# Kernel tuning notes

Hardware: AMD Instinct MI355X
Metric: run time of the kernel (lower is better)

## Reference

```python
import jax, jax.numpy as jnp
import numpy as np

NEG_SLOPE = 0.2  # PyG GATConv default negative_slope


def setup_inputs() -> dict:
    key = jax.random.key(0)
    k_x, k_e, k_w, k_as, k_ad = jax.random.split(key, 5)
    B, F, N, D, E, L = 2, 16, 5000, 128, 40000, 3
    x = jax.random.normal(k_x, (B, F, N, D), dtype=jnp.float32)
    edge_index = jax.random.randint(k_e, (B, F, 2, E), 0, N, dtype=jnp.int64)
    Ws = jax.random.normal(k_w, (L, D, D), dtype=jnp.float32) / np.float32(np.sqrt(D))
    att_src = jax.random.normal(k_as, (L, D), dtype=jnp.float32) / np.float32(np.sqrt(D))
    att_dst = jax.random.normal(k_ad, (L, D), dtype=jnp.float32) / np.float32(np.sqrt(D))
    bias = jnp.zeros((L, D), dtype=jnp.float32)
    return {"x": x, "edge_index": edge_index, "Ws": Ws,
            "att_src": att_src, "att_dst": att_dst, "bias": bias}


def _gat_layer(h, src, dst, n, W, a_s, a_d, b):
    # h: [n, D] node features; src/dst: [E_tot] edge endpoints (self-loops included)
    h2 = h @ W                                   # [n, D] transformed features
    s = h2 @ a_s                                 # [n] per-node source score
    d = h2 @ a_d                                 # [n] per-node dest score
    e = jax.nn.leaky_relu(s[src] + d[dst], NEG_SLOPE)   # [E_tot] raw attention
    m = jax.lax.stop_gradient(jax.ops.segment_max(e, dst, num_segments=n))
    ex = jnp.exp(e - m[dst])                     # numerically stable softmax per dst
    denom = jax.ops.segment_sum(ex, dst, num_segments=n)
    alpha = ex / denom[dst]                      # [E_tot] normalized attention
    out = jax.ops.segment_sum(alpha[:, None] * h2[src], dst, num_segments=n) + b
    return jax.nn.relu(out)


def reference(x, edge_index, Ws, att_src, att_dst, bias):
    B, F, N, D = x.shape
    n = B * F * N
    h = x.reshape(n, D)
    # faithful to torch: (BF,2,E).view(2,-1) is a raw row-major reshape
    ei = edge_index.reshape(2, -1)
    loop = jnp.arange(n, dtype=ei.dtype)         # PyG GATConv adds self-loops
    src = jnp.concatenate([ei[0], loop])
    dst = jnp.concatenate([ei[1], loop])
    for l in range(Ws.shape[0]):                 # fixed small layer loop
        h = _gat_layer(h, src, dst, n, Ws[l], att_src[l], att_dst[l], bias[l])
    return h.reshape(B, F, N, D)
```

## Files before the change

kernel.cpp:

```cpp
#include <hip/hip_runtime.h>
#include <math.h>

#define NODES_TOTAL 160000
#define NODES_REAL  5000
#define D 128
#define NEG 0.2f
#define KP2 128
#define HL2 (128 * KP2)
#define WT2_L (2 * HL2)
#define CHUNK 16384

typedef unsigned short ushort_t;
typedef unsigned int uint_t;
typedef __attribute__((ext_vector_type(8))) __bf16 bf16x8;
typedef __attribute__((ext_vector_type(4))) float f32x4;
union BF8 { bf16x8 v; ushort_t u[8]; };

__device__ __forceinline__ void split2(float x, ushort_t& hi, ushort_t& lo) {
    unsigned u = __float_as_uint(x);
    hi = (ushort_t)(u >> 16);
    float hif = __uint_as_float(u & 0xffff0000u);
    lo = (ushort_t)(__float_as_uint(x - hif) >> 16);
}
__device__ __forceinline__ uint_t encmax(float f) {
    uint_t b = __float_as_uint(f);
    return b ^ ((uint_t)((int)b >> 31) | 0x80000000u);
}
__device__ __forceinline__ float decmax(uint_t u) {
    uint_t b = (u & 0x80000000u) ? (u ^ 0x80000000u) : ~u;
    return __uint_as_float(b);
}

__global__ void wsplit_kernel(const float* __restrict__ Ws, ushort_t* __restrict__ Wm,
                              int* __restrict__ counts, uint_t* __restrict__ gmaxu) {
    int gid = blockIdx.x * 256 + threadIdx.x;
    if (gid < NODES_REAL) counts[gid] = 0;
    if (gid < 3) gmaxu[gid] = 0u;
    int l  = blockIdx.x >> 3;
    int n  = (blockIdx.x & 7) * 16 + (threadIdx.x >> 4);
    int c8 = threadIdx.x & 15;
    int k0 = c8 * 8;
    const float* src = Ws + (size_t)l * D * D;
    union { ushort_t u[8]; uint4 v; } hi, lo;
    #pragma unroll
    for (int j = 0; j < 8; ++j) split2(src[(size_t)(k0 + j) * D + n], hi.u[j], lo.u[j]);
    int ct = n >> 4, m16 = n & 15, kc = c8 >> 2, qq = c8 & 3;
    int lane = qq * 16 + m16;
    ushort_t* d2 = Wm + (size_t)l * WT2_L + ((ct * 4 + kc) * 2 + 0) * 512 + lane * 8;
    *(uint4*)d2 = hi.v;
    *(uint4*)(d2 + 512) = lo.v;
}

__global__ __launch_bounds__(256)
void rank2_kernel(const int* __restrict__ ei, int* __restrict__ counts,
                  int* __restrict__ bases, ushort_t* __restrict__ rank16, int Eh) {
    __shared__ uint_t lc[NODES_REAL];
    int c = blockIdx.x, tid = threadIdx.x;
    for (int i = tid; i < NODES_REAL; i += 256) lc[i] = 0u;
    __syncthreads();
    int e0 = c * CHUNK;
    #pragma unroll 4
    for (int k = 0; k < CHUNK / 256; ++k) {
        int e = e0 + k * 256 + tid;
        if (e < Eh) {
            int d = ei[Eh + e];
            uint_t r = atomicAdd(&lc[d], 1u);
            rank16[e] = (ushort_t)r;
        }
    }
    __syncthreads();
    for (int i = tid; i < NODES_REAL; i += 256) {
        uint_t n = lc[i];
        if (n > 0u)
            bases[c * NODES_REAL + i] = atomicAdd(&counts[i], (int)n);
    }
}

__global__ void scan_kernel(const int* __restrict__ counts, int* __restrict__ offs) {
    __shared__ int sd[1024];
    int t = threadIdx.x;
    int pre[5]; int sum = 0;
    #pragma unroll
    for (int u = 0; u < 5; ++u) {
        int idx = t * 5 + u;
        int c = (idx < NODES_REAL) ? counts[idx] : 0;
        pre[u] = sum; sum += c;
    }
    sd[t] = sum;
    __syncthreads();
    int run = sum;
    for (int o = 1; o < 1024; o <<= 1) {
        int v = (t >= o) ? sd[t - o] : 0;
        __syncthreads();
        sd[t] += v;
        __syncthreads();
    }
    int excl = sd[t] - run;
    #pragma unroll
    for (int u = 0; u < 5; ++u) {
        int idx = t * 5 + u;
        if (idx < NODES_REAL) offs[idx] = excl + pre[u];
    }
    if (t == 1023) offs[NODES_REAL] = excl + run;
}

__global__ void scatter_det(const int* __restrict__ ei, const int* __restrict__ offs,
                            const int* __restrict__ bases,
                            const ushort_t* __restrict__ rank16, ushort_t* __restrict__ esrc,
                            int Eh) {
    int e = blockIdx.x * blockDim.x + threadIdx.x;
    if (e < Eh) {
        int s = ei[e];
        int d = ei[Eh + e];
        int c = e >> 14;
        esrc[offs[d] + bases[c * NODES_REAL + d] + (int)rank16[e]] = (ushort_t)s;
    }
}

__global__ __launch_bounds__(256, 2)
void mlp3_kernel(const float* __restrict__ x, const ushort_t* __restrict__ Wm,
                 const float* __restrict__ bs, float* __restrict__ out) {
    __shared__ float scr[2][2][16][132];
    int tid = threadIdx.x;
    int w = tid >> 6, lane = tid & 63, q = lane >> 4, m16 = lane & 15;
    int p = w >> 1, h = w & 1;
    int row0 = NODES_REAL + blockIdx.x * 64 + p * 32;

    float4 xa[2][4][2];
    #pragma unroll
    for (int rt = 0; rt < 2; ++rt) {
        int r = row0 + rt * 16 + m16;
        if (r > NODES_TOTAL - 1) r = NODES_TOTAL - 1;
        #pragma unroll
        for (int kc = 0; kc < 4; ++kc) {
            const float* gp = x + (size_t)r * D + kc * 32 + q * 8;
            xa[rt][kc][0] = *(const float4*)gp;
            xa[rt][kc][1] = *(const float4*)(gp + 4);
        }
    }

    f32x4 acc[2][4];
    #pragma unroll
    for (int l = 0; l < 3; ++l) {
        const ushort_t* Wml = Wm + (size_t)l * WT2_L;
        if (l > 0) __syncthreads();

        BF8 ahi[2][4], alo[2][4];
        #pragma unroll
        for (int rt = 0; rt < 2; ++rt)
            #pragma unroll
            for (int kc = 0; kc < 4; ++kc) {
                float4 v0, v1;
                if (l == 0) { v0 = xa[rt][kc][0]; v1 = xa[rt][kc][1]; }
                else {
                    const float* sp = &scr[p][rt][m16][kc * 32 + q * 8];
                    v0 = *(const float4*)sp; v1 = *(const float4*)(sp + 4);
                }
                float xv[8] = {v0.x, v0.y, v0.z, v0.w, v1.x, v1.y, v1.z, v1.w};
                #pragma unroll
                for (int j = 0; j < 8; ++j) split2(xv[j], ahi[rt][kc].u[j], alo[rt][kc].u[j]);
            }
        if (l > 0) __syncthreads();

        #pragma unroll
        for (int rt = 0; rt < 2; ++rt)
            #pragma unroll
            for (int ct = 0; ct < 4; ++ct) acc[rt][ct] = (f32x4){0.f, 0.f, 0.f, 0.f};

        #pragma unroll
        for (int ph = 0; ph < 2; ++ph) {
            int kc0 = ph * 2;
            bf16x8 bh[4][2], bl[4][2];
            #pragma unroll
            for (int ct = 0; ct < 4; ++ct)
                #pragma unroll
                for (int dk = 0; dk < 2; ++dk) {
                    const ushort_t* bp = Wml + (((h * 4 + ct) * 4 + (kc0 + dk)) * 2) * 512 + lane * 8;
                    bh[ct][dk] = *(const bf16x8*)bp;
                    bl[ct][dk] = *(const bf16x8*)(bp + 512);
                }
            #pragma unroll
            for (int dk = 0; dk < 2; ++dk)
                #pragma unroll
                for (int ct = 0; ct < 4; ++ct)
                    #pragma unroll
                    for (int rt = 0; rt < 2; ++rt) {
                        acc[rt][ct] = __builtin_amdgcn_mfma_f32_16x16x32_bf16(ahi[rt][kc0 + dk].v, bh[ct][dk], acc[rt][ct], 0, 0, 0);
                        acc[rt][ct] = __builtin_amdgcn_mfma_f32_16x16x32_bf16(ahi[rt][kc0 + dk].v, bl[ct][dk], acc[rt][ct], 0, 0, 0);
                        acc[rt][ct] = __builtin_amdgcn_mfma_f32_16x16x32_bf16(alo[rt][kc0 + dk].v, bh[ct][dk], acc[rt][ct], 0, 0, 0);
                    }
        }
        float bv[4];
        #pragma unroll
        for (int ct = 0; ct < 4; ++ct) bv[ct] = bs[l * D + (h * 4 + ct) * 16 + m16];
        #pragma unroll
        for (int rt = 0; rt < 2; ++rt)
            #pragma unroll
            for (int ct = 0; ct < 4; ++ct)
                #pragma unroll
                for (int reg = 0; reg < 4; ++reg)
                    scr[p][rt][q * 4 + reg][(h * 4 + ct) * 16 + m16] =
                        fmaxf(acc[rt][ct][reg] + bv[ct], 0.f);
    }
    __syncthreads();
    #pragma unroll
    for (int i = 0; i < 8; ++i) {
        int rowl = i * 2 + (lane >> 5);
        int grow = row0 + h * 16 + rowl;
        float4 v = *(const float4*)&scr[p][h][rowl][(lane & 31) * 4];
        if (grow < NODES_TOTAL)
            *(float4*)&out[(size_t)grow * D + (lane & 31) * 4] = v;
    }
}

__global__ __launch_bounds__(64, 2)
void gsmall_kernel(const float* __restrict__ hin, const ushort_t* __restrict__ Wm,
                   const float* __restrict__ a_s, const float* __restrict__ a_d,
                   float* __restrict__ h2, float* __restrict__ sv, float* __restrict__ dv,
                   uint_t* __restrict__ gmaxu) {
    int lane = threadIdx.x & 63, q = lane >> 4, m16 = lane & 15;
    int row0 = blockIdx.x * 16;
    float4 xa[4][2];
    {
        int r = row0 + m16;
        if (r > NODES_REAL - 1) r = NODES_REAL - 1;
        #pragma unroll
        for (int kc = 0; kc < 4; ++kc) {
            const float* gp = hin + (size_t)r * D + kc * 32 + q * 8;
            xa[kc][0] = *(const float4*)gp;
            xa[kc][1] = *(const float4*)(gp + 4);
        }
    }
    f32x4 acc[8];
    #pragma unroll
    for (int ct = 0; ct < 8; ++ct) acc[ct] = (f32x4){0.f, 0.f, 0.f, 0.f};

    #pragma unroll
    for (int kc = 0; kc < 4; ++kc) {
        BF8 ahi, alo;
        {
            float4 v0 = xa[kc][0], v1 = xa[kc][1];
            float xv[8] = {v0.x, v0.y, v0.z, v0.w, v1.x, v1.y, v1.z, v1.w};
            #pragma unroll
            for (int j = 0; j < 8; ++j) split2(xv[j], ahi.u[j], alo.u[j]);
        }
        bf16x8 bh[8], bl[8];
        #pragma unroll
        for (int ct = 0; ct < 8; ++ct) {
            const ushort_t* bp = Wm + ((ct * 4 + kc) * 2) * 512 + lane * 8;
            bh[ct] = *(const bf16x8*)bp;
            bl[ct] = *(const bf16x8*)(bp + 512);
        }
        #pragma unroll
        for (int ct = 0; ct < 8; ++ct) {
            acc[ct] = __builtin_amdgcn_mfma_f32_16x16x32_bf16(ahi.v, bh[ct], acc[ct], 0, 0, 0);
            acc[ct] = __builtin_amdgcn_mfma_f32_16x16x32_bf16(ahi.v, bl[ct], acc[ct], 0, 0, 0);
            acc[ct] = __builtin_amdgcn_mfma_f32_16x16x32_bf16(alo.v, bh[ct], acc[ct], 0, 0, 0);
        }
    }
    #pragma unroll
    for (int reg = 0; reg < 4; ++reg) {
        int grow = row0 + q * 4 + reg;
        if (grow < NODES_REAL) {
            #pragma unroll
            for (int ct = 0; ct < 8; ++ct)
                h2[(size_t)grow * D + ct * 16 + m16] = acc[ct][reg];
        }
    }
    float asv[8], adv[8];
    #pragma unroll
    for (int ct = 0; ct < 8; ++ct) { asv[ct] = a_s[ct * 16 + m16]; adv[ct] = a_d[ct * 16 + m16]; }
    #pragma unroll
    for (int reg = 0; reg < 4; ++reg) {
        float ps = 0.f, pd = 0.f;
        #pragma unroll
        for (int ct = 0; ct < 8; ++ct) {
            float v = acc[ct][reg];
            ps += v * asv[ct]; pd += v * adv[ct];
        }
        #pragma unroll
        for (int o = 1; o < 16; o <<= 1) { ps += __shfl_xor(ps, o); pd += __shfl_xor(pd, o); }
        int grow = row0 + q * 4 + reg;
        if (m16 == 0 && grow < NODES_REAL) {
            sv[grow] = ps; dv[grow] = pd;
            atomicMax(gmaxu, encmax(ps));
        }
    }
}

__global__ __launch_bounds__(256)
void agg_kernel(const float* __restrict__ h2, const float* __restrict__ sv,
                const float* __restrict__ dv, const int* __restrict__ offs,
                const ushort_t* __restrict__ esrc, const float* __restrict__ bias,
                float* __restrict__ out, const uint_t* __restrict__ gmaxu) {
    __shared__ float2 pair_l[512];
    __shared__ float2 red[4][64];
    __shared__ float lexs[4];
    int tid = threadIdx.x, w = tid >> 6, lane = tid & 63;
    int i = blockIdx.x;
    int start = offs[i], end = offs[i + 1];
    float d_i = dv[i];
    float gm = decmax(*gmaxu) + d_i;
    float m = gm > 0.f ? gm : NEG * gm;
    const float2* h2v = (const float2*)h2;
    float ax0 = 0.f, ay0 = 0.f, ax1 = 0.f, ay1 = 0.f;
    float ax2 = 0.f, ay2 = 0.f, ax3 = 0.f, ay3 = 0.f, exs = 0.f;

    for (int tile = start; tile < end; tile += 512) {
        int tcnt = min(512, end - tile);
        __syncthreads();
        #pragma unroll
        for (int hh = 0; hh < 2; ++hh) {
            int j = hh * 256 + tid;
            if (j < tcnt) {
                int s = (int)esrc[tile + j];
                float sc = sv[s] + d_i;
                sc = sc > 0.f ? sc : NEG * sc;
                float ex = __expf(sc - m);
                exs += ex;
                pair_l[j] = make_float2(ex, __uint_as_float((uint_t)s));
            }
        }
        __syncthreads();
        for (int j0 = w * 64; j0 < tcnt; j0 += 256) {
            int jend = min(j0 + 64, tcnt);
            int j = j0;
            for (; j + 4 <= jend; j += 4) {
                float2 p0 = pair_l[j],     p1 = pair_l[j + 1];
                float2 p2 = pair_l[j + 2], p3 = pair_l[j + 3];
                float2 v0 = h2v[(size_t)__float_as_uint(p0.y) * 64 + lane];
                float2 v1 = h2v[(size_t)__float_as_uint(p1.y) * 64 + lane];
                float2 v2 = h2v[(size_t)__float_as_uint(p2.y) * 64 + lane];
                float2 v3 = h2v[(size_t)__float_as_uint(p3.y) * 64 + lane];
                ax0 += p0.x * v0.x; ay0 += p0.x * v0.y;
                ax1 += p1.x * v1.x; ay1 += p1.x * v1.y;
                ax2 += p2.x * v2.x; ay2 += p2.x * v2.y;
                ax3 += p3.x * v3.x; ay3 += p3.x * v3.y;
            }
            for (; j < jend; ++j) {
                float2 p0 = pair_l[j];
                float2 v0 = h2v[(size_t)__float_as_uint(p0.y) * 64 + lane];
                ax0 += p0.x * v0.x; ay0 += p0.x * v0.y;
            }
        }
    }
    float ax = (ax0 + ax1) + (ax2 + ax3);
    float ay = (ay0 + ay1) + (ay2 + ay3);
    #pragma unroll
    for (int o = 1; o < 64; o <<= 1) exs += __shfl_xor(exs, o);
    __syncthreads();
    red[w][lane] = make_float2(ax, ay);
    if (lane == 0) lexs[w] = exs;
    __syncthreads();
    if (w == 0) {
        float2 r1 = red[1][lane], r2 = red[2][lane], r3 = red[3][lane];
        ax += r1.x + r2.x + r3.x;
        ay += r1.y + r2.y + r3.y;
        float exst = lexs[0] + lexs[1] + lexs[2] + lexs[3];
        float scf = sv[i] + d_i; scf = scf > 0.f ? scf : NEG * scf;
        float exf = __expf(scf - m);
        float2 hv = h2v[(size_t)i * 64 + lane];
        ax += exf * hv.x; ay += exf * hv.y;
        float rd = 1.f / (exst + exf);
        float2 b2 = *(const float2*)&bias[2 * lane];
        float2 o2 = make_float2(fmaxf(ax * rd + b2.x, 0.f), fmaxf(ay * rd + b2.y, 0.f));
        *(float2*)&out[(size_t)i * D + 2 * lane] = o2;
    }
}

extern "C" void kernel_launch(void* const* d_in, const int* in_sizes, int n_in,
                              void* d_out, int out_size, void* d_ws, size_t ws_size,
                              hipStream_t stream) {
    const float* x   = (const float*)d_in[0];
    const int*   ei  = (const int*)d_in[1];
    const float* Ws  = (const float*)d_in[2];
    const float* as_ = (const float*)d_in[3];
    const float* ad_ = (const float*)d_in[4];
    const float* bs  = (const float*)d_in[5];
    float* out = (float*)d_out;
    int Eh = in_sizes[1] / 2;
    int nchunks = (Eh + CHUNK - 1) / CHUNK;

    char* ws = (char*)d_ws;
    float*    h2     = (float*)ws;
    float*    bufS   = (float*)(ws + 2560000);
    float*    sv     = (float*)(ws + 5120000);
    float*    dv     = (float*)(ws + 5140000);
    int*      counts = (int*)  (ws + 5160000);
    int*      offs   = (int*)  (ws + 5180000);
    ushort_t* rank16 = (ushort_t*)(ws + 5200016);
    ushort_t* esrc   = (ushort_t*)(ws + 7760016);
    ushort_t* Wm     = (ushort_t*)(ws + 10320016);
    uint_t*   gmaxu  = (uint_t*)(ws + 10528912);
    int*      bases  = (int*)h2;

    wsplit_kernel<<<24, 256, 0, stream>>>(Ws, Wm, counts, gmaxu);
    rank2_kernel<<<nchunks, 256, 0, stream>>>(ei, counts, bases, rank16, Eh);
    scan_kernel<<<1, 1024, 0, stream>>>(counts, offs);
    scatter_det<<<(Eh + 255) / 256, 256, 0, stream>>>(ei, offs, bases, rank16, esrc, Eh);

    mlp3_kernel<<<(NODES_TOTAL - NODES_REAL + 63) / 64, 256, 0, stream>>>(x, Wm, bs, out);

    for (int l = 0; l < 3; ++l) {
        const float* hin = (l == 0) ? x : bufS;
        float* hout = (l == 2) ? out : bufS;
        gsmall_kernel<<<(NODES_REAL + 15) / 16, 64, 0, stream>>>(
            hin, Wm + (size_t)l * WT2_L, as_ + l * D, ad_ + l * D, h2, sv, dv, gmaxu + l);
        agg_kernel<<<NODES_REAL, 256, 0, stream>>>(
            h2, sv, dv, offs, esrc, bs + l * D, hout, gmaxu + l);
    }
}
```

Before: 481.2 us.

## Fuse graph build and three GAT layers into a persistent grid-synced megakernel

Replaces the separate rank, scan, scatter, per-layer transform and aggregation launches with one persistent kernel of 1024 blocks. The phases are separated by a software grid barrier built on a global atomic counter. Layer-0 feature transform now runs alongside the CSR ranking phase. The aim is to remove launch gaps and kernel tails across about ten small dependent kernels. In exchange it depends on all 1024 blocks being resident at once, because otherwise the spin barrier deadlocks, and it adds barrier spin cost.

```diff
diff --git a/kernel.cpp b/kernel.cpp
--- a/kernel.cpp
+++ b/kernel.cpp
@@ -9,6 +9,7 @@
 #define HL2 (128 * KP2)
 #define WT2_L (2 * HL2)
 #define CHUNK 16384
+#define MEGA_NB 1024
 
 typedef unsigned short ushort_t;
 typedef unsigned int uint_t;
@@ -31,11 +32,24 @@
     return __uint_as_float(b);
 }
 
+__device__ __forceinline__ void grid_sync(uint_t* cnt, uint_t target) {
+    __syncthreads();
+    if (threadIdx.x == 0) {
+        __threadfence();
+        atomicAdd(cnt, 1u);
+        while (*(volatile uint_t*)cnt < target) __builtin_amdgcn_s_sleep(2);
+        __threadfence();
+    }
+    __syncthreads();
+}
+
 __global__ void wsplit_kernel(const float* __restrict__ Ws, ushort_t* __restrict__ Wm,
-                              int* __restrict__ counts, uint_t* __restrict__ gmaxu) {
+                              int* __restrict__ counts, uint_t* __restrict__ gmaxu,
+                              uint_t* __restrict__ sync_cnt) {
     int gid = blockIdx.x * 256 + threadIdx.x;
     if (gid < NODES_REAL) counts[gid] = 0;
     if (gid < 3) gmaxu[gid] = 0u;
+    if (gid == 3) *sync_cnt = 0u;
     int l  = blockIdx.x >> 3;
     int n  = (blockIdx.x & 7) * 16 + (threadIdx.x >> 4);
     int c8 = threadIdx.x & 15;
@@ -49,72 +63,6 @@
     ushort_t* d2 = Wm + (size_t)l * WT2_L + ((ct * 4 + kc) * 2 + 0) * 512 + lane * 8;
     *(uint4*)d2 = hi.v;
     *(uint4*)(d2 + 512) = lo.v;
-}
-
-__global__ __launch_bounds__(256)
-void rank2_kernel(const int* __restrict__ ei, int* __restrict__ counts,
-                  int* __restrict__ bases, ushort_t* __restrict__ rank16, int Eh) {
-    __shared__ uint_t lc[NODES_REAL];
-    int c = blockIdx.x, tid = threadIdx.x;
-    for (int i = tid; i < NODES_REAL; i += 256) lc[i] = 0u;
-    __syncthreads();
-    int e0 = c * CHUNK;
-    #pragma unroll 4
-    for (int k = 0; k < CHUNK / 256; ++k) {
-        int e = e0 + k * 256 + tid;
-        if (e < Eh) {
-            int d = ei[Eh + e];
-            uint_t r = atomicAdd(&lc[d], 1u);
-            rank16[e] = (ushort_t)r;
-        }
-    }
-    __syncthreads();
-    for (int i = tid; i < NODES_REAL; i += 256) {
-        uint_t n = lc[i];
-        if (n > 0u)
-            bases[c * NODES_REAL + i] = atomicAdd(&counts[i], (int)n);
-    }
-}
-
-__global__ void scan_kernel(const int* __restrict__ counts, int* __restrict__ offs) {
-    __shared__ int sd[1024];
-    int t = threadIdx.x;
-    int pre[5]; int sum = 0;
-    #pragma unroll
-    for (int u = 0; u < 5; ++u) {
-        int idx = t * 5 + u;
-        int c = (idx < NODES_REAL) ? counts[idx] : 0;
-        pre[u] = sum; sum += c;
-    }
-    sd[t] = sum;
-    __syncthreads();
-    int run = sum;
-    for (int o = 1; o < 1024; o <<= 1) {
-        int v = (t >= o) ? sd[t - o] : 0;
-        __syncthreads();
-        sd[t] += v;
-        __syncthreads();
-    }
-    int excl = sd[t] - run;
-    #pragma unroll
-    for (int u = 0; u < 5; ++u) {
-        int idx = t * 5 + u;
-        if (idx < NODES_REAL) offs[idx] = excl + pre[u];
-    }
-    if (t == 1023) offs[NODES_REAL] = excl + run;
-}
-
-__global__ void scatter_det(const int* __restrict__ ei, const int* __restrict__ offs,
-                            const int* __restrict__ bases,
-                            const ushort_t* __restrict__ rank16, ushort_t* __restrict__ esrc,
-                            int Eh) {
-    int e = blockIdx.x * blockDim.x + threadIdx.x;
-    if (e < Eh) {
-        int s = ei[e];
-        int d = ei[Eh + e];
-        int c = e >> 14;
-        esrc[offs[d] + bases[c * NODES_REAL + d] + (int)rank16[e]] = (ushort_t)s;
-    }
 }
 
 __global__ __launch_bounds__(256, 2)
@@ -213,49 +161,43 @@
     }
 }
 
-__global__ __launch_bounds__(64, 2)
-void gsmall_kernel(const float* __restrict__ hin, const ushort_t* __restrict__ Wm,
-                   const float* __restrict__ a_s, const float* __restrict__ a_d,
-                   float* __restrict__ h2, float* __restrict__ sv, float* __restrict__ dv,
-                   uint_t* __restrict__ gmaxu) {
-    int lane = threadIdx.x & 63, q = lane >> 4, m16 = lane & 15;
-    int row0 = blockIdx.x * 16;
-    float4 xa[4][2];
-    {
-        int r = row0 + m16;
-        if (r > NODES_REAL - 1) r = NODES_REAL - 1;
-        #pragma unroll
-        for (int kc = 0; kc < 4; ++kc) {
-            const float* gp = hin + (size_t)r * D + kc * 32 + q * 8;
-            xa[kc][0] = *(const float4*)gp;
-            xa[kc][1] = *(const float4*)(gp + 4);
-        }
-    }
+__device__ __forceinline__ void gsmall_wave(const float* __restrict__ hin,
+        const ushort_t* __restrict__ Wml, const float* __restrict__ a_s,
+        const float* __restrict__ a_d, float* __restrict__ h2,
+        float* __restrict__ sv, float* __restrict__ dv, uint_t* __restrict__ gmax,
+        int row0, int lane) {
+    int q = lane >> 4, m16 = lane & 15;
+    int rr = row0 + m16; if (rr > NODES_REAL - 1) rr = NODES_REAL - 1;
     f32x4 acc[8];
     #pragma unroll
     for (int ct = 0; ct < 8; ++ct) acc[ct] = (f32x4){0.f, 0.f, 0.f, 0.f};
-
     #pragma unroll
     for (int kc = 0; kc < 4; ++kc) {
+        const float* gp = hin + (size_t)rr * D + kc * 32 + q * 8;
+        float4 v0 = *(const float4*)gp, v1 = *(const float4*)(gp + 4);
         BF8 ahi, alo;
         {
-            float4 v0 = xa[kc][0], v1 = xa[kc][1];
             float xv[8] = {v0.x, v0.y, v0.z, v0.w, v1.x, v1.y, v1.z, v1.w};
             #pragma unroll
             for (int j = 0; j < 8; ++j) split2(xv[j], ahi.u[j], alo.u[j]);
         }
-        bf16x8 bh[8], bl[8];
-        #pragma unroll
-        for (int ct = 0; ct < 8; ++ct) {
-            const ushort_t* bp = Wm + ((ct * 4 + kc) * 2) * 512 + lane * 8;
-            bh[ct] = *(const bf16x8*)bp;
-            bl[ct] = *(const bf16x8*)(bp + 512);
-        }
-        #pragma unroll
-        for (int ct = 0; ct < 8; ++ct) {
-            acc[ct] = __builtin_amdgcn_mfma_f32_16x16x32_bf16(ahi.v, bh[ct], acc[ct], 0, 0, 0);
-            acc[ct] = __builtin_amdgcn_mfma_f32_16x16x32_bf16(ahi.v, bl[ct], acc[ct], 0, 0, 0);
-            acc[ct] = __builtin_amdgcn_mfma_f32_16x16x32_bf16(alo.v, bh[ct], acc[ct], 0, 0, 0);
+        #pragma unroll
+        for (int cth = 0; cth < 2; ++cth) {
+            bf16x8 bh[4], bl[4];
+            #pragma unroll
+            for (int c4 = 0; c4 < 4; ++c4) {
+                int ct = cth * 4 + c4;
+                const ushort_t* bp = Wml + ((ct * 4 + kc) * 2) * 512 + lane * 8;
+                bh[c4] = *(const bf16x8*)bp;
+                bl[c4] = *(const bf16x8*)(bp + 512);
+            }
+            #pragma unroll
+            for (int c4 = 0; c4 < 4; ++c4) {
+                int ct = cth * 4 + c4;
+                acc[ct] = __builtin_amdgcn_mfma_f32_16x16x32_bf16(ahi.v, bh[c4], acc[ct], 0, 0, 0);
+                acc[ct] = __builtin_amdgcn_mfma_f32_16x16x32_bf16(ahi.v, bl[c4], acc[ct], 0, 0, 0);
+                acc[ct] = __builtin_amdgcn_mfma_f32_16x16x32_bf16(alo.v, bh[c4], acc[ct], 0, 0, 0);
+            }
         }
     }
     #pragma unroll
@@ -283,21 +225,17 @@
         int grow = row0 + q * 4 + reg;
         if (m16 == 0 && grow < NODES_REAL) {
             sv[grow] = ps; dv[grow] = pd;
-            atomicMax(gmaxu, encmax(ps));
-        }
-    }
-}
-
-__global__ __launch_bounds__(256)
-void agg_kernel(const float* __restrict__ h2, const float* __restrict__ sv,
-                const float* __restrict__ dv, const int* __restrict__ offs,
-                const ushort_t* __restrict__ esrc, const float* __restrict__ bias,
-                float* __restrict__ out, const uint_t* __restrict__ gmaxu) {
-    __shared__ float2 pair_l[512];
-    __shared__ float2 red[4][64];
-    __shared__ float lexs[4];
-    int tid = threadIdx.x, w = tid >> 6, lane = tid & 63;
-    int i = blockIdx.x;
+            atomicMax(gmax, encmax(ps));
+        }
+    }
+}
+
+__device__ __forceinline__ void agg_dst(int i, const float* __restrict__ h2,
+        const float* __restrict__ sv, const float* __restrict__ dv,
+        const int* __restrict__ offs, const ushort_t* __restrict__ esrc,
+        const float* __restrict__ bias, float* __restrict__ hout,
+        const uint_t* __restrict__ gmaxu, int w, int lane, int tid,
+        float2* pair_l, float2 (*red)[64], float* lexs) {
     int start = offs[i], end = offs[i + 1];
     float d_i = dv[i];
     float gm = decmax(*gmaxu) + d_i;
@@ -305,7 +243,6 @@
     const float2* h2v = (const float2*)h2;
     float ax0 = 0.f, ay0 = 0.f, ax1 = 0.f, ay1 = 0.f;
     float ax2 = 0.f, ay2 = 0.f, ax3 = 0.f, ay3 = 0.f, exs = 0.f;
-
     for (int tile = start; tile < end; tile += 512) {
         int tcnt = min(512, end - tile);
         __syncthreads();
@@ -364,8 +301,116 @@
         float rd = 1.f / (exst + exf);
         float2 b2 = *(const float2*)&bias[2 * lane];
         float2 o2 = make_float2(fmaxf(ax * rd + b2.x, 0.f), fmaxf(ay * rd + b2.y, 0.f));
-        *(float2*)&out[(size_t)i * D + 2 * lane] = o2;
-    }
+        *(float2*)&hout[(size_t)i * D + 2 * lane] = o2;
+    }
+}
+
+__global__ __launch_bounds__(256, 4)
+void mega_kernel(const float* __restrict__ x, const ushort_t* __restrict__ Wm,
+                 const float* __restrict__ as_, const float* __restrict__ ad_,
+                 const float* __restrict__ bs, const int* __restrict__ ei,
+                 float* __restrict__ h2, float* __restrict__ bufS,
+                 float* __restrict__ sv, float* __restrict__ dv,
+                 int* __restrict__ counts, int* __restrict__ offs,
+                 ushort_t* __restrict__ rank16, ushort_t* __restrict__ esrc,
+                 uint_t* __restrict__ gmaxu, float* __restrict__ out,
+                 uint_t* __restrict__ sync_cnt, int Eh, int nchunks) {
+    __shared__ uint_t lc[NODES_REAL];
+    __shared__ float2 pair_l[512];
+    __shared__ float2 red[4][64];
+    __shared__ float lexs[4];
+    __shared__ int sd2[256];
+    int b = blockIdx.x, tid = threadIdx.x;
+    int w = tid >> 6, lane = tid & 63;
+    uint_t NB = gridDim.x;
+    int* bases = (int*)bufS;
+
+    if (b < nchunks) {
+        for (int i2 = tid; i2 < NODES_REAL; i2 += 256) lc[i2] = 0u;
+        __syncthreads();
+        int e0 = b * CHUNK;
+        #pragma unroll 4
+        for (int k = 0; k < CHUNK / 256; ++k) {
+            int e = e0 + k * 256 + tid;
+            if (e < Eh) {
+                int d = ei[Eh + e];
+                uint_t r = atomicAdd(&lc[d], 1u);
+                rank16[e] = (ushort_t)r;
+            }
+        }
+        __syncthreads();
+        for (int i2 = tid; i2 < NODES_REAL; i2 += 256) {
+            uint_t n = lc[i2];
+            if (n > 0u)
+                bases[b * NODES_REAL + i2] = atomicAdd(&counts[i2], (int)n);
+        }
+    } else {
+        int gw = (b - nchunks) * 4 + w;
+        if (gw * 16 < NODES_REAL)
+            gsmall_wave(x, Wm, as_, ad_, h2, sv, dv, gmaxu + 0, gw * 16, lane);
+    }
+    uint_t tgt = NB; grid_sync(sync_cnt, tgt);
+
+    if (b == 0) {
+        int t = tid;
+        int pre[20]; int sum = 0;
+        #pragma unroll
+        for (int u = 0; u < 20; ++u) {
+            int idx = t * 20 + u;
+            int c = (idx < NODES_REAL) ? counts[idx] : 0;
+            pre[u] = sum; sum += c;
+        }
+        sd2[t] = sum;
+        __syncthreads();
+        int run = sum;
+        for (int o = 1; o < 256; o <<= 1) {
+            int v = (t >= o) ? sd2[t - o] : 0;
+            __syncthreads();
+            sd2[t] += v;
+            __syncthreads();
+        }
+        int excl = sd2[t] - run;
+        #pragma unroll
+        for (int u = 0; u < 20; ++u) {
+            int idx = t * 20 + u;
+            if (idx < NODES_REAL) offs[idx] = excl + pre[u];
+        }
+        if (t == 255) offs[NODES_REAL] = excl + run;
+    }
+    tgt += NB; grid_sync(sync_cnt, tgt);
+
+    for (int e = b * 256 + tid; e < Eh; e += (int)NB * 256) {
+        int s = ei[e];
+        int d = ei[Eh + e];
+        int c = e >> 14;
+        esrc[offs[d] + bases[c * NODES_REAL + d] + (int)rank16[e]] = (ushort_t)s;
+    }
+    tgt += NB; grid_sync(sync_cnt, tgt);
+
+    for (int i = b; i < NODES_REAL; i += (int)NB)
+        agg_dst(i, h2, sv, dv, offs, esrc, bs + 0 * D, bufS, gmaxu + 0, w, lane, tid, pair_l, red, lexs);
+    tgt += NB; grid_sync(sync_cnt, tgt);
+
+    {
+        int gw = b * 4 + w;
+        if (gw * 16 < NODES_REAL)
+            gsmall_wave(bufS, Wm + WT2_L, as_ + D, ad_ + D, h2, sv, dv, gmaxu + 1, gw * 16, lane);
+    }
+    tgt += NB; grid_sync(sync_cnt, tgt);
+
+    for (int i = b; i < NODES_REAL; i += (int)NB)
+        agg_dst(i, h2, sv, dv, offs, esrc, bs + D, bufS, gmaxu + 1, w, lane, tid, pair_l, red, lexs);
+    tgt += NB; grid_sync(sync_cnt, tgt);
+
+    {
+        int gw = b * 4 + w;
+        if (gw * 16 < NODES_REAL)
+            gsmall_wave(bufS, Wm + 2 * WT2_L, as_ + 2 * D, ad_ + 2 * D, h2, sv, dv, gmaxu + 2, gw * 16, lane);
+    }
+    tgt += NB; grid_sync(sync_cnt, tgt);
+
+    for (int i = b; i < NODES_REAL; i += (int)NB)
+        agg_dst(i, h2, sv, dv, offs, esrc, bs + 2 * D, out, gmaxu + 2, w, lane, tid, pair_l, red, lexs);
 }
 
 extern "C" void kernel_launch(void* const* d_in, const int* in_sizes, int n_in,
@@ -392,21 +437,13 @@
     ushort_t* esrc   = (ushort_t*)(ws + 7760016);
     ushort_t* Wm     = (ushort_t*)(ws + 10320016);
     uint_t*   gmaxu  = (uint_t*)(ws + 10528912);
-    int*      bases  = (int*)h2;
-
-    wsplit_kernel<<<24, 256, 0, stream>>>(Ws, Wm, counts, gmaxu);
-    rank2_kernel<<<nchunks, 256, 0, stream>>>(ei, counts, bases, rank16, Eh);
-    scan_kernel<<<1, 1024, 0, stream>>>(counts, offs);
-    scatter_det<<<(Eh + 255) / 256, 256, 0, stream>>>(ei, offs, bases, rank16, esrc, Eh);
+    uint_t*   sync_cnt = (uint_t*)(ws + 10528928);
+
+    wsplit_kernel<<<24, 256, 0, stream>>>(Ws, Wm, counts, gmaxu, sync_cnt);
 
     mlp3_kernel<<<(NODES_TOTAL - NODES_REAL + 63) / 64, 256, 0, stream>>>(x, Wm, bs, out);
 
-    for (int l = 0; l < 3; ++l) {
-        const float* hin = (l == 0) ? x : bufS;
-        float* hout = (l == 2) ? out : bufS;
-        gsmall_kernel<<<(NODES_REAL + 15) / 16, 64, 0, stream>>>(
-            hin, Wm + (size_t)l * WT2_L, as_ + l * D, ad_ + l * D, h2, sv, dv, gmaxu + l);
-        agg_kernel<<<NODES_REAL, 256, 0, stream>>>(
-            h2, sv, dv, offs, esrc, bs + l * D, hout, gmaxu + l);
-    }
-}
+    mega_kernel<<<MEGA_NB, 256, 0, stream>>>(x, Wm, as_, ad_, bs, ei, h2, bufS, sv, dv,
+                                             counts, offs, rank16, esrc, gmaxu, out,
+                                             sync_cnt, Eh, nchunks);
+}
```

New measurement: 1.429 ms. 2.97x slower.

## Overlap MLP for isolated nodes with graph layers via combined kernels

Applied to the files above, without the earlier changes.

The large MLP over nodes without edges is split into three slices, and each slice is launched in the same grid as one layer's aggregation blocks. This lets the independent dense work fill the GPU while the latency-bound per-node aggregation runs. The edge-rank kernel is also merged with the layer-0 feature transform, and the rank bases buffer moves to bufS so it does not clash with h2. The cost is higher LDS and register use in the merged kernels, which may lower occupancy, and the blocks become unevenly sized.

```diff
diff --git a/kernel.cpp b/kernel.cpp
--- a/kernel.cpp
+++ b/kernel.cpp
@@ -51,80 +51,13 @@
     *(uint4*)(d2 + 512) = lo.v;
 }
 
-__global__ __launch_bounds__(256)
-void rank2_kernel(const int* __restrict__ ei, int* __restrict__ counts,
-                  int* __restrict__ bases, ushort_t* __restrict__ rank16, int Eh) {
-    __shared__ uint_t lc[NODES_REAL];
-    int c = blockIdx.x, tid = threadIdx.x;
-    for (int i = tid; i < NODES_REAL; i += 256) lc[i] = 0u;
-    __syncthreads();
-    int e0 = c * CHUNK;
-    #pragma unroll 4
-    for (int k = 0; k < CHUNK / 256; ++k) {
-        int e = e0 + k * 256 + tid;
-        if (e < Eh) {
-            int d = ei[Eh + e];
-            uint_t r = atomicAdd(&lc[d], 1u);
-            rank16[e] = (ushort_t)r;
-        }
-    }
-    __syncthreads();
-    for (int i = tid; i < NODES_REAL; i += 256) {
-        uint_t n = lc[i];
-        if (n > 0u)
-            bases[c * NODES_REAL + i] = atomicAdd(&counts[i], (int)n);
-    }
-}
-
-__global__ void scan_kernel(const int* __restrict__ counts, int* __restrict__ offs) {
-    __shared__ int sd[1024];
-    int t = threadIdx.x;
-    int pre[5]; int sum = 0;
-    #pragma unroll
-    for (int u = 0; u < 5; ++u) {
-        int idx = t * 5 + u;
-        int c = (idx < NODES_REAL) ? counts[idx] : 0;
-        pre[u] = sum; sum += c;
-    }
-    sd[t] = sum;
-    __syncthreads();
-    int run = sum;
-    for (int o = 1; o < 1024; o <<= 1) {
-        int v = (t >= o) ? sd[t - o] : 0;
-        __syncthreads();
-        sd[t] += v;
-        __syncthreads();
-    }
-    int excl = sd[t] - run;
-    #pragma unroll
-    for (int u = 0; u < 5; ++u) {
-        int idx = t * 5 + u;
-        if (idx < NODES_REAL) offs[idx] = excl + pre[u];
-    }
-    if (t == 1023) offs[NODES_REAL] = excl + run;
-}
-
-__global__ void scatter_det(const int* __restrict__ ei, const int* __restrict__ offs,
-                            const int* __restrict__ bases,
-                            const ushort_t* __restrict__ rank16, ushort_t* __restrict__ esrc,
-                            int Eh) {
-    int e = blockIdx.x * blockDim.x + threadIdx.x;
-    if (e < Eh) {
-        int s = ei[e];
-        int d = ei[Eh + e];
-        int c = e >> 14;
-        esrc[offs[d] + bases[c * NODES_REAL + d] + (int)rank16[e]] = (ushort_t)s;
-    }
-}
-
-__global__ __launch_bounds__(256, 2)
-void mlp3_kernel(const float* __restrict__ x, const ushort_t* __restrict__ Wm,
-                 const float* __restrict__ bs, float* __restrict__ out) {
-    __shared__ float scr[2][2][16][132];
-    int tid = threadIdx.x;
+__device__ __forceinline__ void mlp3_body(const float* __restrict__ x,
+        const ushort_t* __restrict__ Wm, const float* __restrict__ bs,
+        float* __restrict__ out, int row_base, int bid, int tid,
+        float (*scr)[2][16][132]) {
     int w = tid >> 6, lane = tid & 63, q = lane >> 4, m16 = lane & 15;
     int p = w >> 1, h = w & 1;
-    int row0 = NODES_REAL + blockIdx.x * 64 + p * 32;
+    int row0 = row_base + bid * 64 + p * 32;
 
     float4 xa[2][4][2];
     #pragma unroll
@@ -213,49 +146,43 @@
     }
 }
 
-__global__ __launch_bounds__(64, 2)
-void gsmall_kernel(const float* __restrict__ hin, const ushort_t* __restrict__ Wm,
-                   const float* __restrict__ a_s, const float* __restrict__ a_d,
-                   float* __restrict__ h2, float* __restrict__ sv, float* __restrict__ dv,
-                   uint_t* __restrict__ gmaxu) {
-    int lane = threadIdx.x & 63, q = lane >> 4, m16 = lane & 15;
-    int row0 = blockIdx.x * 16;
-    float4 xa[4][2];
-    {
-        int r = row0 + m16;
-        if (r > NODES_REAL - 1) r = NODES_REAL - 1;
-        #pragma unroll
-        for (int kc = 0; kc < 4; ++kc) {
-            const float* gp = hin + (size_t)r * D + kc * 32 + q * 8;
-            xa[kc][0] = *(const float4*)gp;
-            xa[kc][1] = *(const float4*)(gp + 4);
-        }
-    }
+__device__ __forceinline__ void gsmall_wave(const float* __restrict__ hin,
+        const ushort_t* __restrict__ Wml, const float* __restrict__ a_s,
+        const float* __restrict__ a_d, float* __restrict__ h2,
+        float* __restrict__ sv, float* __restrict__ dv, uint_t* __restrict__ gmax,
+        int row0, int lane) {
+    int q = lane >> 4, m16 = lane & 15;
+    int rr = row0 + m16; if (rr > NODES_REAL - 1) rr = NODES_REAL - 1;
     f32x4 acc[8];
     #pragma unroll
     for (int ct = 0; ct < 8; ++ct) acc[ct] = (f32x4){0.f, 0.f, 0.f, 0.f};
-
     #pragma unroll
     for (int kc = 0; kc < 4; ++kc) {
+        const float* gp = hin + (size_t)rr * D + kc * 32 + q * 8;
+        float4 v0 = *(const float4*)gp, v1 = *(const float4*)(gp + 4);
         BF8 ahi, alo;
         {
-            float4 v0 = xa[kc][0], v1 = xa[kc][1];
             float xv[8] = {v0.x, v0.y, v0.z, v0.w, v1.x, v1.y, v1.z, v1.w};
             #pragma unroll
             for (int j = 0; j < 8; ++j) split2(xv[j], ahi.u[j], alo.u[j]);
         }
-        bf16x8 bh[8], bl[8];
-        #pragma unroll
-        for (int ct = 0; ct < 8; ++ct) {
-            const ushort_t* bp = Wm + ((ct * 4 + kc) * 2) * 512 + lane * 8;
-            bh[ct] = *(const bf16x8*)bp;
-            bl[ct] = *(const bf16x8*)(bp + 512);
-        }
-        #pragma unroll
-        for (int ct = 0; ct < 8; ++ct) {
-            acc[ct] = __builtin_amdgcn_mfma_f32_16x16x32_bf16(ahi.v, bh[ct], acc[ct], 0, 0, 0);
-            acc[ct] = __builtin_amdgcn_mfma_f32_16x16x32_bf16(ahi.v, bl[ct], acc[ct], 0, 0, 0);
-            acc[ct] = __builtin_amdgcn_mfma_f32_16x16x32_bf16(alo.v, bh[ct], acc[ct], 0, 0, 0);
+        #pragma unroll
+        for (int cth = 0; cth < 2; ++cth) {
+            bf16x8 bh[4], bl[4];
+            #pragma unroll
+            for (int c4 = 0; c4 < 4; ++c4) {
+                int ct = cth * 4 + c4;
+                const ushort_t* bp = Wml + ((ct * 4 + kc) * 2) * 512 + lane * 8;
+                bh[c4] = *(const bf16x8*)bp;
+                bl[c4] = *(const bf16x8*)(bp + 512);
+            }
+            #pragma unroll
+            for (int c4 = 0; c4 < 4; ++c4) {
+                int ct = cth * 4 + c4;
+                acc[ct] = __builtin_amdgcn_mfma_f32_16x16x32_bf16(ahi.v, bh[c4], acc[ct], 0, 0, 0);
+                acc[ct] = __builtin_amdgcn_mfma_f32_16x16x32_bf16(ahi.v, bl[c4], acc[ct], 0, 0, 0);
+                acc[ct] = __builtin_amdgcn_mfma_f32_16x16x32_bf16(alo.v, bh[c4], acc[ct], 0, 0, 0);
+            }
         }
     }
     #pragma unroll
@@ -283,21 +210,17 @@
         int grow = row0 + q * 4 + reg;
         if (m16 == 0 && grow < NODES_REAL) {
             sv[grow] = ps; dv[grow] = pd;
-            atomicMax(gmaxu, encmax(ps));
-        }
-    }
-}
-
-__global__ __launch_bounds__(256)
-void agg_kernel(const float* __restrict__ h2, const float* __restrict__ sv,
-                const float* __restrict__ dv, const int* __restrict__ offs,
-                const ushort_t* __restrict__ esrc, const float* __restrict__ bias,
-                float* __restrict__ out, const uint_t* __restrict__ gmaxu) {
-    __shared__ float2 pair_l[512];
-    __shared__ float2 red[4][64];
-    __shared__ float lexs[4];
-    int tid = threadIdx.x, w = tid >> 6, lane = tid & 63;
-    int i = blockIdx.x;
+            atomicMax(gmax, encmax(ps));
+        }
+    }
+}
+
+__device__ __forceinline__ void agg_dst(int i, const float* __restrict__ h2,
+        const float* __restrict__ sv, const float* __restrict__ dv,
+        const int* __restrict__ offs, const ushort_t* __restrict__ esrc,
+        const float* __restrict__ bias, float* __restrict__ hout,
+        const uint_t* __restrict__ gmaxu, int w, int lane, int tid,
+        float2* pair_l, float2 (*red)[64], float* lexs) {
     int start = offs[i], end = offs[i + 1];
     float d_i = dv[i];
     float gm = decmax(*gmaxu) + d_i;
@@ -305,7 +228,6 @@
     const float2* h2v = (const float2*)h2;
     float ax0 = 0.f, ay0 = 0.f, ax1 = 0.f, ay1 = 0.f;
     float ax2 = 0.f, ay2 = 0.f, ax3 = 0.f, ay3 = 0.f, exs = 0.f;
-
     for (int tile = start; tile < end; tile += 512) {
         int tcnt = min(512, end - tile);
         __syncthreads();
@@ -364,8 +286,115 @@
         float rd = 1.f / (exst + exf);
         float2 b2 = *(const float2*)&bias[2 * lane];
         float2 o2 = make_float2(fmaxf(ax * rd + b2.x, 0.f), fmaxf(ay * rd + b2.y, 0.f));
-        *(float2*)&out[(size_t)i * D + 2 * lane] = o2;
-    }
+        *(float2*)&hout[(size_t)i * D + 2 * lane] = o2;
+    }
+}
+
+__global__ __launch_bounds__(256, 4)
+void comboA_kernel(const int* __restrict__ ei, int* __restrict__ counts,
+                   int* __restrict__ bases, ushort_t* __restrict__ rank16,
+                   int Eh, int nchunks,
+                   const float* __restrict__ x, const ushort_t* __restrict__ Wm,
+                   const float* __restrict__ as_, const float* __restrict__ ad_,
+                   float* __restrict__ h2, float* __restrict__ sv,
+                   float* __restrict__ dv, uint_t* __restrict__ gmaxu) {
+    __shared__ uint_t lc[NODES_REAL];
+    int b = blockIdx.x, tid = threadIdx.x;
+    if (b < nchunks) {
+        for (int i2 = tid; i2 < NODES_REAL; i2 += 256) lc[i2] = 0u;
+        __syncthreads();
+        int e0 = b * CHUNK;
+        #pragma unroll 4
+        for (int k = 0; k < CHUNK / 256; ++k) {
+            int e = e0 + k * 256 + tid;
+            if (e < Eh) {
+                int d = ei[Eh + e];
+                uint_t r = atomicAdd(&lc[d], 1u);
+                rank16[e] = (ushort_t)r;
+            }
+        }
+        __syncthreads();
+        for (int i2 = tid; i2 < NODES_REAL; i2 += 256) {
+            uint_t n = lc[i2];
+            if (n > 0u)
+                bases[b * NODES_REAL + i2] = atomicAdd(&counts[i2], (int)n);
+        }
+    } else {
+        int gw = (b - nchunks) * 4 + (tid >> 6);
+        if (gw * 16 < NODES_REAL)
+            gsmall_wave(x, Wm, as_, ad_, h2, sv, dv, gmaxu + 0, gw * 16, tid & 63);
+    }
+}
+
+__global__ void scan_kernel(const int* __restrict__ counts, int* __restrict__ offs) {
+    __shared__ int sd[1024];
+    int t = threadIdx.x;
+    int pre[5]; int sum = 0;
+    #pragma unroll
+    for (int u = 0; u < 5; ++u) {
+        int idx = t * 5 + u;
+        int c = (idx < NODES_REAL) ? counts[idx] : 0;
+        pre[u] = sum; sum += c;
+    }
+    sd[t] = sum;
+    __syncthreads();
+    int run = sum;
+    for (int o = 1; o < 1024; o <<= 1) {
+        int v = (t >= o) ? sd[t - o] : 0;
+        __syncthreads();
+        sd[t] += v;
+        __syncthreads();
+    }
+    int excl = sd[t] - run;
+    #pragma unroll
+    for (int u = 0; u < 5; ++u) {
+        int idx = t * 5 + u;
+        if (idx < NODES_REAL) offs[idx] = excl + pre[u];
+    }
+    if (t == 1023) offs[NODES_REAL] = excl + run;
+}
+
+__global__ void scatter_det(const int* __restrict__ ei, const int* __restrict__ offs,
+                            const int* __restrict__ bases,
+                            const ushort_t* __restrict__ rank16, ushort_t* __restrict__ esrc,
+                            int Eh) {
+    int e = blockIdx.x * blockDim.x + threadIdx.x;
+    if (e < Eh) {
+        int s = ei[e];
+        int d = ei[Eh + e];
+        int c = e >> 14;
+        esrc[offs[d] + bases[c * NODES_REAL + d] + (int)rank16[e]] = (ushort_t)s;
+    }
+}
+
+__global__ __launch_bounds__(256, 2)
+void combo_kernel(const float* __restrict__ x, const ushort_t* __restrict__ Wm,
+                  const float* __restrict__ bs, float* __restrict__ out,
+                  int mlp_nb, int mlp_row_base,
+                  const float* __restrict__ h2, const float* __restrict__ sv,
+                  const float* __restrict__ dv, const int* __restrict__ offs,
+                  const ushort_t* __restrict__ esrc, const float* __restrict__ bias_l,
+                  float* __restrict__ hout, const uint_t* __restrict__ gmaxu_l) {
+    __shared__ float scr[2][2][16][132];
+    __shared__ float2 pair_l[512];
+    __shared__ float2 red[4][64];
+    __shared__ float lexs[4];
+    int b = blockIdx.x, tid = threadIdx.x;
+    if (b < mlp_nb) {
+        mlp3_body(x, Wm, bs, out, mlp_row_base, b, tid, scr);
+    } else {
+        int i = b - mlp_nb;
+        agg_dst(i, h2, sv, dv, offs, esrc, bias_l, hout, gmaxu_l,
+                tid >> 6, tid & 63, tid, pair_l, red, lexs);
+    }
+}
+
+__global__ __launch_bounds__(64, 2)
+void gsmall_kernel(const float* __restrict__ hin, const ushort_t* __restrict__ Wm,
+                   const float* __restrict__ a_s, const float* __restrict__ a_d,
+                   float* __restrict__ h2, float* __restrict__ sv, float* __restrict__ dv,
+                   uint_t* __restrict__ gmaxu) {
+    gsmall_wave(hin, Wm, a_s, a_d, h2, sv, dv, gmaxu, blockIdx.x * 16, threadIdx.x & 63);
 }
 
 extern "C" void kernel_launch(void* const* d_in, const int* in_sizes, int n_in,
@@ -392,21 +421,28 @@
     ushort_t* esrc   = (ushort_t*)(ws + 7760016);
     ushort_t* Wm     = (ushort_t*)(ws + 10320016);
     uint_t*   gmaxu  = (uint_t*)(ws + 10528912);
-    int*      bases  = (int*)h2;
+    int*      bases  = (int*)bufS;
+
+    const int MLP_NB = (NODES_TOTAL - NODES_REAL + 63) / 64;
+    const int S0 = 808, S1 = 808, S2 = MLP_NB - S0 - S1;
 
     wsplit_kernel<<<24, 256, 0, stream>>>(Ws, Wm, counts, gmaxu);
-    rank2_kernel<<<nchunks, 256, 0, stream>>>(ei, counts, bases, rank16, Eh);
+    comboA_kernel<<<nchunks + (NODES_REAL + 63) / 64, 256, 0, stream>>>(
+        ei, counts, bases, rank16, Eh, nchunks, x, Wm, as_, ad_, h2, sv, dv, gmaxu);
     scan_kernel<<<1, 1024, 0, stream>>>(counts, offs);
     scatter_det<<<(Eh + 255) / 256, 256, 0, stream>>>(ei, offs, bases, rank16, esrc, Eh);
 
-    mlp3_kernel<<<(NODES_TOTAL - NODES_REAL + 63) / 64, 256, 0, stream>>>(x, Wm, bs, out);
-
-    for (int l = 0; l < 3; ++l) {
-        const float* hin = (l == 0) ? x : bufS;
-        float* hout = (l == 2) ? out : bufS;
-        gsmall_kernel<<<(NODES_REAL + 15) / 16, 64, 0, stream>>>(
-            hin, Wm + (size_t)l * WT2_L, as_ + l * D, ad_ + l * D, h2, sv, dv, gmaxu + l);
-        agg_kernel<<<NODES_REAL, 256, 0, stream>>>(
-            h2, sv, dv, offs, esrc, bs + l * D, hout, gmaxu + l);
-    }
-}
+    combo_kernel<<<S0 + NODES_REAL, 256, 0, stream>>>(
+        x, Wm, bs, out, S0, NODES_REAL + 0 * 64,
+        h2, sv, dv, offs, esrc, bs + 0 * D, bufS, gmaxu + 0);
+    gsmall_kernel<<<(NODES_REAL + 15) / 16, 64, 0, stream>>>(
+        bufS, Wm + WT2_L, as_ + D, ad_ + D, h2, sv, dv, gmaxu + 1);
+    combo_kernel<<<S1 + NODES_REAL, 256, 0, stream>>>(
+        x, Wm, bs, out, S1, NODES_REAL + S0 * 64,
+        h2, sv, dv, offs, esrc, bs + 1 * D, bufS, gmaxu + 1);
+    gsmall_kernel<<<(NODES_REAL + 15) / 16, 64, 0, stream>>>(
+        bufS, Wm + 2 * WT2_L, as_ + 2 * D, ad_ + 2 * D, h2, sv, dv, gmaxu + 2);
+    combo_kernel<<<S2 + NODES_REAL, 256, 0, stream>>>(
+        x, Wm, bs, out, S2, NODES_REAL + (S0 + S1) * 64,
+        h2, sv, dv, offs, esrc, bs + 2 * D, out, gmaxu + 2);
+}
```

Result: no change. 477.7 us (-0.7%).
